# Kernel tuning notes

Hardware: AMD Instinct MI355X
Metric: run time of the kernel (lower is better)

## Reference

```python
import jax, jax.numpy as jnp
import numpy as np

EPS_LN = 1e-5

def _layernorm(x, g, b):
    mu = jnp.mean(x, axis=-1, keepdims=True)
    var = jnp.mean((x - mu) ** 2, axis=-1, keepdims=True)
    return (x - mu) * jax.lax.rsqrt(var + EPS_LN) * g + b

def _act_quant_ste(x):
    # clip_val uses detached stats -> stop_gradient
    clip_val = jax.lax.stop_gradient(
        jnp.clip(jnp.mean(jnp.abs(x), axis=-1, keepdims=True), 1e-8, None)) * 2.5
    scale = clip_val / 127.0
    x_scaled = x / scale
    x_clip = jnp.clip(x_scaled, -127.0, 127.0)
    x_q = x_scaled + jax.lax.stop_gradient(jnp.round(x_clip) - x_scaled)
    return x_q * scale

def _weight_quant_ste(w):
    scale = jax.lax.stop_gradient(jnp.clip(jnp.mean(jnp.abs(w)), 1e-8, None))
    w_norm = w / scale
    w_clip = jnp.clip(w_norm, -1.0, 1.0)
    w_q = w_norm + jax.lax.stop_gradient(jnp.round(w_clip) - w_norm)
    return w_q * scale

def _bitlinear(x, w, g, b):
    # w: [out, in]; x: [B,T,in]
    x_q = _act_quant_ste(_layernorm(x, g, b))
    w_q = _weight_quant_ste(w)
    return jnp.einsum('btd,hd->bth', x_q, w_q)

def setup_inputs() -> dict:
    D, H = 2048, 2048 * 4
    B, T = 4, 2048
    key = jax.random.key(0)
    ks = jax.random.split(key, 4)
    std = 0.02
    return {
        'x': jax.random.normal(ks[0], (B, T, D), dtype=jnp.float32),
        'mu_k': jnp.zeros((1, 1, D), jnp.float32),
        'mu_r': jnp.zeros((1, 1, D), jnp.float32),
        'wk': jax.random.normal(ks[1], (H, D), jnp.float32) * std,
        'gk': jnp.ones((D,), jnp.float32), 'bk': jnp.zeros((D,), jnp.float32),
        'wr': jax.random.normal(ks[2], (D, D), jnp.float32) * std,
        'gr': jnp.ones((D,), jnp.float32), 'br': jnp.zeros((D,), jnp.float32),
        'wv': jax.random.normal(ks[3], (D, H), jnp.float32) * std,
        'gv': jnp.ones((H,), jnp.float32), 'bv': jnp.zeros((H,), jnp.float32),
    }

def reference(x, mu_k, mu_r, wk, gk, bk, wr, gr, br, wv, gv, bv):
    B, T, C = x.shape
    prev = jnp.zeros((B, 1, C), dtype=x.dtype)  # state=None path
    x_prev = jnp.concatenate([prev, x[:, :-1, :]], axis=1)  # token shift
    dx = x_prev - x
    k_act = jax.nn.relu(_bitlinear(x + dx * mu_k, wk, gk, bk)) ** 2  # [B,T,H]
    rgate = jax.nn.sigmoid(_bitlinear(x + dx * mu_r, wr, gr, br))    # [B,T,D]
    out = rgate * _bitlinear(k_act, wv, gv, bv)                      # [B,T,D]
    return out, jax.lax.stop_gradient(x[:, -1:, :])
```

## Files before the change

### kernel.cpp

```cpp
#include <hip/hip_runtime.h>

#define T_LEN 2048
#define B_SZ  4
#define D_DIM 2048
#define H_DIM 8192
#define BT    (B_SZ * T_LEN)

typedef float f32x4 __attribute__((ext_vector_type(4)));
typedef int   i32x4v __attribute__((ext_vector_type(4)));
typedef int   i32x16v __attribute__((ext_vector_type(16)));
typedef unsigned short ushort8 __attribute__((ext_vector_type(8)));

__device__ __forceinline__ float bf2f(unsigned short u) {
    unsigned int i = ((unsigned int)u) << 16;
    return __builtin_bit_cast(float, i);
}
__device__ __forceinline__ unsigned short f2bf(float f) {
    unsigned int i = __builtin_bit_cast(unsigned int, f);
    i += 0x7fffu + ((i >> 16) & 1u);
    return (unsigned short)(i >> 16);
}

__device__ __forceinline__ float block_sum(float v, float* red) {
    #pragma unroll
    for (int o = 32; o > 0; o >>= 1) v += __shfl_down(v, o, 64);
    const int lane = threadIdx.x & 63, w = threadIdx.x >> 6;
    if (lane == 0) red[w] = v;
    __syncthreads();
    float r = red[0] + red[1] + red[2] + red[3];
    __syncthreads();
    return r;
}

__global__ void wabs_all(const float* __restrict__ wk, const float* __restrict__ wr,
                         const float* __restrict__ wv, float* __restrict__ part) {
    __shared__ float red[16];
    const int m = blockIdx.x >> 10;
    const int blk = blockIdx.x & 1023;
    const float* w = (m == 0) ? wk : (m == 1) ? wr : wv;
    const int n = (m == 1) ? D_DIM * D_DIM : H_DIM * D_DIM;
    float s = 0.f;
    int i = (blk * 256 + threadIdx.x) * 8;
    const int stride = 1024 * 256 * 8;
    for (; i < n; i += stride) {
        f32x4 a = *(const f32x4*)(w + i);
        f32x4 b = *(const f32x4*)(w + i + 4);
        #pragma unroll
        for (int j = 0; j < 4; j++) s += fabsf(a[j]) + fabsf(b[j]);
    }
    float tot = block_sum(s, red);
    if (threadIdx.x == 0) part[blockIdx.x] = tot;
}

__global__ void wfinal_all(const float* __restrict__ part, float* __restrict__ wsc) {
    __shared__ float red[16];
    const int m = blockIdx.x;
    const int n = (m == 1) ? D_DIM * D_DIM : H_DIM * D_DIM;
    float s = 0.f;
    for (int i = threadIdx.x; i < 1024; i += 256) s += part[m * 1024 + i];
    float tot = block_sum(s, red);
    if (threadIdx.x == 0) wsc[m] = fmaxf(tot / (float)n, 1e-8f);
}

__global__ void wquant_all(const float* __restrict__ wk, const float* __restrict__ wr,
                           const float* __restrict__ wv,
                           signed char* __restrict__ qk, signed char* __restrict__ qr,
                           signed char* __restrict__ qv,
                           const float* __restrict__ wsc) {
    const int b = blockIdx.x;
    int m, blk, nblk;
    if (b < 2048)      { m = 0; blk = b;        nblk = 2048; }
    else if (b < 3072) { m = 1; blk = b - 2048; nblk = 1024; }
    else               { m = 2; blk = b - 3072; nblk = 2048; }
    const float* w = (m == 0) ? wk : (m == 1) ? wr : wv;
    signed char* q = (m == 0) ? qk : (m == 1) ? qr : qv;
    const int n = (m == 1) ? D_DIM * D_DIM : H_DIM * D_DIM;
    const float s = wsc[m];
    int i = (blk * 256 + threadIdx.x) * 16;
    const int stride = nblk * 256 * 16;
    for (; i < n; i += stride) {
        union { signed char c[16]; i32x4v v; } pk;
        #pragma unroll
        for (int h = 0; h < 4; h++) {
            f32x4 a = *(const f32x4*)(w + i + h * 4);
            #pragma unroll
            for (int j = 0; j < 4; j++)
                pk.c[h * 4 + j] =
                    (signed char)(int)rintf(fminf(fmaxf(a[j] / s, -1.f), 1.f));
        }
        *(i32x4v*)(q + i) = pk.v;
    }
}

__device__ __forceinline__ void ln_quant8(const float* xm_in,
                                          const float* __restrict__ g,
                                          const float* __restrict__ b,
                                          signed char* qrow, float* srow, float* red) {
    const int base = threadIdx.x * 8;
    float xm[8];
    float s = 0.f;
    #pragma unroll
    for (int j = 0; j < 8; j++) { xm[j] = xm_in[j]; s += xm[j]; }
    const float mean = block_sum(s, red) * (1.f / D_DIM);
    float s2 = 0.f;
    #pragma unroll
    for (int j = 0; j < 8; j++) { float d = xm[j] - mean; s2 += d * d; }
    const float var  = block_sum(s2, red) * (1.f / D_DIM);
    const float rstd = 1.f / sqrtf(var + 1e-5f);
    f32x4 ga = *(const f32x4*)(g + base), gb = *(const f32x4*)(g + base + 4);
    f32x4 ba = *(const f32x4*)(b + base), bb2 = *(const f32x4*)(b + base + 4);
    float gg[8] = {ga[0],ga[1],ga[2],ga[3],gb[0],gb[1],gb[2],gb[3]};
    float bb[8] = {ba[0],ba[1],ba[2],ba[3],bb2[0],bb2[1],bb2[2],bb2[3]};
    float sa = 0.f;
    #pragma unroll
    for (int j = 0; j < 8; j++) {
        xm[j] = (xm[j] - mean) * rstd * gg[j] + bb[j];
        sa += fabsf(xm[j]);
    }
    const float amean = block_sum(sa, red) * (1.f / D_DIM);
    const float scale = fmaxf(amean, 1e-8f) * 2.5f / 127.0f;
    union { signed char c[8]; int2 v; } pk;
    #pragma unroll
    for (int j = 0; j < 8; j++)
        pk.c[j] = (signed char)(int)rintf(fminf(fmaxf(xm[j] / scale, -127.f), 127.f));
    *(int2*)(qrow + base) = pk.v;
    if (threadIdx.x == 0) *srow = scale;
}

__global__ void act_prep(const float* __restrict__ x,
                         const float* __restrict__ muk,
                         const float* __restrict__ gk, const float* __restrict__ bk,
                         const float* __restrict__ mur,
                         const float* __restrict__ gr, const float* __restrict__ br,
                         signed char* __restrict__ qk, float* __restrict__ sk,
                         signed char* __restrict__ qr, float* __restrict__ sr,
                         float* __restrict__ out2) {
    __shared__ float red[16];
    const int row = blockIdx.x;
    const int t = row & (T_LEN - 1);
    const int base = threadIdx.x * 8;

    float xv[8], xp[8];
    f32x4 xa = *(const f32x4*)(x + (size_t)row * D_DIM + base);
    f32x4 xb = *(const f32x4*)(x + (size_t)row * D_DIM + base + 4);
    xv[0]=xa[0]; xv[1]=xa[1]; xv[2]=xa[2]; xv[3]=xa[3];
    xv[4]=xb[0]; xv[5]=xb[1]; xv[6]=xb[2]; xv[7]=xb[3];
    if (t > 0) {
        f32x4 pa = *(const f32x4*)(x + (size_t)(row - 1) * D_DIM + base);
        f32x4 pb = *(const f32x4*)(x + (size_t)(row - 1) * D_DIM + base + 4);
        xp[0]=pa[0]; xp[1]=pa[1]; xp[2]=pa[2]; xp[3]=pa[3];
        xp[4]=pb[0]; xp[5]=pb[1]; xp[6]=pb[2]; xp[7]=pb[3];
    } else {
        #pragma unroll
        for (int j = 0; j < 8; j++) xp[j] = 0.f;
    }
    if (t == T_LEN - 1) {
        const int bb = row / T_LEN;
        *(f32x4*)(out2 + (size_t)bb * D_DIM + base)     = xa;
        *(f32x4*)(out2 + (size_t)bb * D_DIM + base + 4) = xb;
    }
    float mk[8], mr[8], xmk[8], xmr[8];
    f32x4 mka = *(const f32x4*)(muk + base), mkb = *(const f32x4*)(muk + base + 4);
    f32x4 mra = *(const f32x4*)(mur + base), mrb = *(const f32x4*)(mur + base + 4);
    mk[0]=mka[0]; mk[1]=mka[1]; mk[2]=mka[2]; mk[3]=mka[3];
    mk[4]=mkb[0]; mk[5]=mkb[1]; mk[6]=mkb[2]; mk[7]=mkb[3];
    mr[0]=mra[0]; mr[1]=mra[1]; mr[2]=mra[2]; mr[3]=mra[3];
    mr[4]=mrb[0]; mr[5]=mrb[1]; mr[6]=mrb[2]; mr[7]=mrb[3];
    #pragma unroll
    for (int j = 0; j < 8; j++) {
        const float dx = xp[j] - xv[j];
        xmk[j] = xv[j] + dx * mk[j];
        xmr[j] = xv[j] + dx * mr[j];
    }
    ln_quant8(xmk, gk, bk, qk + (size_t)row * D_DIM, sk + row, red);
    ln_quant8(xmr, gr, br, qr + (size_t)row * D_DIM, sr + row, red);
}

__global__ void lnq_v(const unsigned short* __restrict__ kact,
                      const float* __restrict__ g, const float* __restrict__ b,
                      signed char* __restrict__ qv, float* __restrict__ sv) {
    __shared__ float red[16];
    const int row = blockIdx.x;
    const int base = threadIdx.x * 32;
    const unsigned short* kr = kact + (size_t)row * H_DIM + base;

    float v[32];
    float s = 0.f;
    #pragma unroll
    for (int c = 0; c < 4; c++) {
        ushort8 a = *(const ushort8*)(kr + c * 8);
        #pragma unroll
        for (int j = 0; j < 8; j++) { v[c * 8 + j] = bf2f(a[j]); s += v[c * 8 + j]; }
    }
    const float mean = block_sum(s, red) * (1.f / H_DIM);
    float s2 = 0.f;
    #pragma unroll
    for (int j = 0; j < 32; j++) { float d = v[j] - mean; s2 += d * d; }
    const float var  = block_sum(s2, red) * (1.f / H_DIM);
    const float rstd = 1.f / sqrtf(var + 1e-5f);
    float sa = 0.f;
    #pragma unroll
    for (int c = 0; c < 8; c++) {
        f32x4 ga = *(const f32x4*)(g + base + c * 4);
        f32x4 ba = *(const f32x4*)(b + base + c * 4);
        #pragma unroll
        for (int j = 0; j < 4; j++) {
            int k = c * 4 + j;
            v[k] = (v[k] - mean) * rstd * ga[j] + ba[j];
            sa += fabsf(v[k]);
        }
    }
    const float amean = block_sum(sa, red) * (1.f / H_DIM);
    const float scale = fmaxf(amean, 1e-8f) * 2.5f / 127.0f;
    union { signed char c[32]; i32x4v v4[2]; } pk;
    #pragma unroll
    for (int j = 0; j < 32; j++)
        pk.c[j] = (signed char)(int)rintf(fminf(fmaxf(v[j] / scale, -127.f), 127.f));
    *(i32x4v*)(qv + (size_t)row * H_DIM + base)      = pk.v4[0];
    *(i32x4v*)(qv + (size_t)row * H_DIM + base + 16) = pk.v4[1];
    if (threadIdx.x == 0) sv[row] = scale;
}

template <int EP, int MT>
__global__ __launch_bounds__(512, 2) void gemmR(
    const signed char* __restrict__ A, const signed char* __restrict__ B,
    int K, int Nn, int gn,
    const float* __restrict__ sa, const float* __restrict__ swp,
    const unsigned short* __restrict__ gate_bf, float* __restrict__ out_f,
    unsigned short* __restrict__ out_bf) {
    constexpr int BM = MT * 256;
    __shared__ signed char Bs[4][128 * 64];
    const int tid = threadIdx.x;
    const int nwg = gridDim.x, q8 = nwg >> 3;
    const int swz = (blockIdx.x & 7) * q8 + (blockIdx.x >> 3);
    const int bm = swz / gn, bn = swz % gn;
    const int lane = tid & 63, wave = tid >> 6;
    const int lrow = lane & 31, lhalf = lane >> 5;
    const size_t arow0 = (size_t)bm * BM;
    const size_t brow0 = (size_t)bn * 128;
    const int NT = K >> 6;

    i32x16v acc[MT][4] = {};

    auto stageB = [&](int buf, int k0) {
        const int r = tid >> 2, sl = tid & 3;
        const signed char* g = B + (brow0 + r) * (size_t)K + k0 + ((sl ^ ((r >> 1) & 3)) * 16);
        __builtin_amdgcn_global_load_lds(
            (const __attribute__((address_space(1))) void*)g,
            (__attribute__((address_space(3))) void*)(Bs[buf] + tid * 16), 16, 0, 0);
    };
    auto loadA = [&](i32x4v (&a)[MT][2], int k0) {
        #pragma unroll
        for (int tm = 0; tm < MT; tm++)
            #pragma unroll
            for (int s = 0; s < 2; s++) {
                const int r = wave * (MT * 32) + tm * 32 + lrow;
                a[tm][s] = *(const i32x4v*)(A + (arow0 + r) * (size_t)K + k0 + (s * 2 + lhalf) * 16);
            }
    };
    auto readB = [&](const signed char* BsB, i32x4v (&b)[4][2]) {
        #pragma unroll
        for (int s = 0; s < 2; s++) {
            const int slot = s * 2 + lhalf;
            #pragma unroll
            for (int tn = 0; tn < 4; tn++) {
                const int r = tn * 32 + lrow;
                b[tn][s] = *(const i32x4v*)(BsB + r * 64 + ((slot ^ ((r >> 1) & 3)) * 16));
            }
        }
    };
    auto mfmaT = [&](i32x4v (&a)[MT][2], i32x4v (&b)[4][2]) {
        #pragma unroll
        for (int s = 0; s < 2; s++)
            #pragma unroll
            for (int tm = 0; tm < MT; tm++)
                #pragma unroll
                for (int tn = 0; tn < 4; tn++)
                    acc[tm][tn] = __builtin_amdgcn_mfma_i32_32x32x32_i8(
                        a[tm][s], b[tn][s], acc[tm][tn], 0, 0, 0);
    };

    i32x4v aE[MT][2], aO[MT][2];
    stageB(0, 0);
    loadA(aE, 0);
    stageB(1, 64);

    auto body = [&](int t, i32x4v (&cur)[MT][2], i32x4v (&nxt)[MT][2]) {
        const bool hasA = (t + 1 < NT);
        const bool hasB = (t + 2 < NT);
        if (hasA) loadA(nxt, (t + 1) << 6);
        if (hasB) stageB((t + 2) & 3, (t + 2) << 6);
        if (hasB) {
            if constexpr (MT == 2) asm volatile("s_waitcnt vmcnt(6)" ::: "memory");
            else                   asm volatile("s_waitcnt vmcnt(4)" ::: "memory");
        } else if (hasA) {
            if constexpr (MT == 2) asm volatile("s_waitcnt vmcnt(5)" ::: "memory");
            else                   asm volatile("s_waitcnt vmcnt(3)" ::: "memory");
        } else {
            asm volatile("s_waitcnt vmcnt(0)" ::: "memory");
        }
        __builtin_amdgcn_sched_barrier(0);
        __builtin_amdgcn_s_barrier();
        {
            i32x4v b[4][2];
            readB(Bs[t & 3], b);
            __builtin_amdgcn_s_setprio(1);
            mfmaT(cur, b);
            __builtin_amdgcn_s_setprio(0);
        }
    };

    for (int t = 0; t < NT; t += 2) {
        body(t, aE, aO);
        body(t + 1, aO, aE);
    }

    const float sw = *swp;
    #pragma unroll
    for (int tm = 0; tm < MT; tm++) {
        #pragma unroll
        for (int tn = 0; tn < 4; tn++) {
            #pragma unroll
            for (int rg = 0; rg < 16; rg++) {
                const int rin  = (rg & 3) + 8 * (rg >> 2) + 4 * lhalf;
                const int grow = bm * BM + wave * (MT * 32) + tm * 32 + rin;
                const int gcol = bn * 128 + tn * 32 + lrow;
                const float v = (float)acc[tm][tn][rg] * sa[grow] * sw;
                const size_t idx = (size_t)grow * Nn + gcol;
                if (EP == 0) {
                    float rv = fmaxf(v, 0.f);
                    out_bf[idx] = f2bf(rv * rv);
                } else if (EP == 1) {
                    out_bf[idx] = f2bf(1.0f / (1.0f + expf(-v)));
                } else {
                    out_f[idx] = bf2f(gate_bf[idx]) * v;
                }
            }
        }
    }
}

extern "C" void kernel_launch(void* const* d_in, const int* in_sizes, int n_in,
                              void* d_out, int out_size, void* d_ws, size_t ws_size,
                              hipStream_t stream) {
    const float* x   = (const float*)d_in[0];
    const float* muk = (const float*)d_in[1];
    const float* mur = (const float*)d_in[2];
    const float* wk  = (const float*)d_in[3];
    const float* gk  = (const float*)d_in[4];
    const float* bk  = (const float*)d_in[5];
    const float* wr  = (const float*)d_in[6];
    const float* gr  = (const float*)d_in[7];
    const float* br  = (const float*)d_in[8];
    const float* wv  = (const float*)d_in[9];
    const float* gv  = (const float*)d_in[10];
    const float* bv  = (const float*)d_in[11];

    char* wsb = (char*)d_ws;
    size_t off = 0;
    auto alloc = [&](size_t bytes) -> size_t {
        size_t p = off;
        off = (off + bytes + 255) & ~(size_t)255;
        return p;
    };
    const size_t o_wqk  = alloc((size_t)H_DIM * D_DIM);
    const size_t o_wqr  = alloc((size_t)D_DIM * D_DIM);
    const size_t o_wqv  = alloc((size_t)D_DIM * H_DIM);
    const size_t o_wsc  = alloc(64);
    const size_t o_part = alloc(3 * 1024 * sizeof(float));
    const size_t o_xqk  = alloc((size_t)BT * D_DIM);
    const size_t o_xqr  = alloc((size_t)BT * D_DIM);
    const size_t o_gate = alloc((size_t)BT * D_DIM * 2);
    const size_t o_sk   = alloc((size_t)BT * 4);
    const size_t o_sr   = alloc((size_t)BT * 4);
    const size_t fixed  = off;

    int CH = BT;
    while (CH > 512 &&
           fixed + (size_t)CH * (H_DIM + 2 * H_DIM + 4) + 8192 > ws_size)
        CH >>= 1;
    const size_t o_xqv  = alloc((size_t)CH * H_DIM);
    const size_t o_kact = alloc((size_t)CH * H_DIM * 2);
    const size_t o_sv   = alloc((size_t)CH * 4);

    signed char* wqk = (signed char*)(wsb + o_wqk);
    signed char* wqr = (signed char*)(wsb + o_wqr);
    signed char* wqv = (signed char*)(wsb + o_wqv);
    float* wsc  = (float*)(wsb + o_wsc);
    float* part = (float*)(wsb + o_part);
    signed char* xqk = (signed char*)(wsb + o_xqk);
    signed char* xqr = (signed char*)(wsb + o_xqr);
    unsigned short* gate = (unsigned short*)(wsb + o_gate);
    float* sk = (float*)(wsb + o_sk);
    float* sr = (float*)(wsb + o_sr);
    signed char* xqv = (signed char*)(wsb + o_xqv);
    unsigned short* kact = (unsigned short*)(wsb + o_kact);
    float* sv = (float*)(wsb + o_sv);

    float* outp = (float*)d_out;
    float* out2 = outp + (size_t)BT * D_DIM;

    wabs_all<<<3072, 256, 0, stream>>>(wk, wr, wv, part);
    wfinal_all<<<3, 256, 0, stream>>>(part, wsc);
    wquant_all<<<5120, 256, 0, stream>>>(wk, wr, wv, wqk, wqr, wqv, wsc);

    act_prep<<<BT, 256, 0, stream>>>(x, muk, gk, bk, mur, gr, br,
                                     xqk, sk, xqr, sr, out2);

    gemmR<1, 1><<<(BT / 256) * (D_DIM / 128), 512, 0, stream>>>(
        xqr, wqr, D_DIM, D_DIM, D_DIM / 128, sr, wsc + 1,
        (const unsigned short*)nullptr, (float*)nullptr, gate);

    for (int row0 = 0; row0 < BT; row0 += CH) {
        gemmR<0, 2><<<(CH / 512) * (H_DIM / 128), 512, 0, stream>>>(
            xqk + (size_t)row0 * D_DIM, wqk, D_DIM, H_DIM, H_DIM / 128,
            sk + row0, wsc + 0,
            (const unsigned short*)nullptr, (float*)nullptr, kact);

        lnq_v<<<CH, 256, 0, stream>>>(kact, gv, bv, xqv, sv);

        gemmR<2, 1><<<(CH / 256) * (D_DIM / 128), 512, 0, stream>>>(
            xqv, wqv, H_DIM, D_DIM, D_DIM / 128, sv, wsc + 2,
            gate + (size_t)row0 * D_DIM, outp + (size_t)row0 * D_DIM,
            (unsigned short*)nullptr);
    }
}
```

Measured before the change: 674.0 us.

## Pre-tile int8 activations for MFMA fragments and deepen GEMM K pipeline

The activation quantizers now write int8 activations into a tiled layout of 32-row by 16-byte blocks, so each GEMM wave loads its A fragments as fully contiguous 512-byte chunks instead of strided row reads. The GEMM is rewritten to stage 256-wide K slices of B into a triple-buffered shared-memory ring, prefetching the next slice and A fragments while computing the current one. The M tile drops to 256 rows for all three GEMMs, including the large K-projection that previously used 512. This cuts per-iteration barriers and improves A load coalescing, but uses more LDS per block, which may reduce occupancy, and loses the larger M tile's reuse of B for the big GEMM.

```diff
diff --git a/kernel.cpp b/kernel.cpp
--- a/kernel.cpp
+++ b/kernel.cpp
@@ -95,7 +95,8 @@
 __device__ __forceinline__ void ln_quant8(const float* xm_in,
                                           const float* __restrict__ g,
                                           const float* __restrict__ b,
-                                          signed char* qrow, float* srow, float* red) {
+                                          signed char* qbase, int row,
+                                          float* srow, float* red) {
     const int base = threadIdx.x * 8;
     float xm[8];
     float s = 0.f;
@@ -123,7 +124,9 @@
     #pragma unroll
     for (int j = 0; j < 8; j++)
         pk.c[j] = (signed char)(int)rintf(fminf(fmaxf(xm[j] / scale, -127.f), 127.f));
-    *(int2*)(qrow + base) = pk.v;
+    const size_t addr = ((size_t)(row >> 5) * (D_DIM / 16) + (threadIdx.x >> 1)) * 512
+                        + (row & 31) * 16 + (threadIdx.x & 1) * 8;
+    *(int2*)(qbase + addr) = pk.v;
     if (threadIdx.x == 0) *srow = scale;
 }
 
@@ -172,8 +175,8 @@
         xmk[j] = xv[j] + dx * mk[j];
         xmr[j] = xv[j] + dx * mr[j];
     }
-    ln_quant8(xmk, gk, bk, qk + (size_t)row * D_DIM, sk + row, red);
-    ln_quant8(xmr, gr, br, qr + (size_t)row * D_DIM, sr + row, red);
+    ln_quant8(xmk, gk, bk, qk, row, sk + row, red);
+    ln_quant8(xmr, gr, br, qr, row, sr + row, red);
 }
 
 __global__ void lnq_v(const unsigned short* __restrict__ kact,
@@ -216,125 +219,120 @@
     #pragma unroll
     for (int j = 0; j < 32; j++)
         pk.c[j] = (signed char)(int)rintf(fminf(fmaxf(v[j] / scale, -127.f), 127.f));
-    *(i32x4v*)(qv + (size_t)row * H_DIM + base)      = pk.v4[0];
-    *(i32x4v*)(qv + (size_t)row * H_DIM + base + 16) = pk.v4[1];
+    const size_t tb = ((size_t)(row >> 5) * (H_DIM / 16) + threadIdx.x * 2) * 512
+                      + (row & 31) * 16;
+    *(i32x4v*)(qv + tb)       = pk.v4[0];
+    *(i32x4v*)(qv + tb + 512) = pk.v4[1];
     if (threadIdx.x == 0) sv[row] = scale;
 }
 
-template <int EP, int MT>
-__global__ __launch_bounds__(512, 2) void gemmR(
-    const signed char* __restrict__ A, const signed char* __restrict__ B,
+template <int EP>
+__global__ __launch_bounds__(512, 2) void gemmP(
+    const signed char* __restrict__ Ap, const signed char* __restrict__ B,
     int K, int Nn, int gn,
     const float* __restrict__ sa, const float* __restrict__ swp,
     const unsigned short* __restrict__ gate_bf, float* __restrict__ out_f,
     unsigned short* __restrict__ out_bf) {
-    constexpr int BM = MT * 256;
-    __shared__ signed char Bs[4][128 * 64];
+    __shared__ signed char Bs[3 * 32768];
     const int tid = threadIdx.x;
     const int nwg = gridDim.x, q8 = nwg >> 3;
     const int swz = (blockIdx.x & 7) * q8 + (blockIdx.x >> 3);
     const int bm = swz / gn, bn = swz % gn;
     const int lane = tid & 63, wave = tid >> 6;
     const int lrow = lane & 31, lhalf = lane >> 5;
-    const size_t arow0 = (size_t)bm * BM;
+    const int KS = K >> 4;
+    const size_t rts = (size_t)(bm * 8 + wave) * KS;
     const size_t brow0 = (size_t)bn * 128;
-    const int NT = K >> 6;
-
-    i32x16v acc[MT][4] = {};
-
-    auto stageB = [&](int buf, int k0) {
+    const int NB = K >> 8;
+
+    i32x16v acc[4] = {};
+
+    auto stageB = [&](int p, int t) {
         const int r = tid >> 2, sl = tid & 3;
-        const signed char* g = B + (brow0 + r) * (size_t)K + k0 + ((sl ^ ((r >> 1) & 3)) * 16);
-        __builtin_amdgcn_global_load_lds(
-            (const __attribute__((address_space(1))) void*)g,
-            (__attribute__((address_space(3))) void*)(Bs[buf] + tid * 16), 16, 0, 0);
+        #pragma unroll
+        for (int j = 0; j < 4; j++) {
+            const signed char* g = B + (brow0 + r) * (size_t)K + (t * 256 + j * 64)
+                                   + ((sl ^ ((r >> 1) & 3)) * 16);
+            __builtin_amdgcn_global_load_lds(
+                (const __attribute__((address_space(1))) void*)g,
+                (__attribute__((address_space(3))) void*)(Bs + p * 32768 + j * 8192 + tid * 16),
+                16, 0, 0);
+        }
     };
-    auto loadA = [&](i32x4v (&a)[MT][2], int k0) {
-        #pragma unroll
-        for (int tm = 0; tm < MT; tm++)
+    auto loadA = [&](i32x4v (&a)[4][2], int t) {
+        #pragma unroll
+        for (int s = 0; s < 4; s++)
             #pragma unroll
-            for (int s = 0; s < 2; s++) {
-                const int r = wave * (MT * 32) + tm * 32 + lrow;
-                a[tm][s] = *(const i32x4v*)(A + (arow0 + r) * (size_t)K + k0 + (s * 2 + lhalf) * 16);
-            }
+            for (int sl = 0; sl < 2; sl++)
+                a[s][sl] = *(const i32x4v*)(
+                    Ap + ((rts + (size_t)(t * 16 + s * 4 + sl * 2)) << 9) + lane * 16);
     };
-    auto readB = [&](const signed char* BsB, i32x4v (&b)[4][2]) {
-        #pragma unroll
-        for (int s = 0; s < 2; s++) {
-            const int slot = s * 2 + lhalf;
+    auto readB = [&](int p, int s, i32x4v (&b)[4][2]) {
+        const signed char* basep = Bs + p * 32768 + s * 8192;
+        #pragma unroll
+        for (int sl = 0; sl < 2; sl++) {
+            const int slot = sl * 2 + lhalf;
             #pragma unroll
             for (int tn = 0; tn < 4; tn++) {
                 const int r = tn * 32 + lrow;
-                b[tn][s] = *(const i32x4v*)(BsB + r * 64 + ((slot ^ ((r >> 1) & 3)) * 16));
+                b[tn][sl] = *(const i32x4v*)(basep + r * 64 + ((slot ^ ((r >> 1) & 3)) * 16));
             }
         }
     };
-    auto mfmaT = [&](i32x4v (&a)[MT][2], i32x4v (&b)[4][2]) {
-        #pragma unroll
-        for (int s = 0; s < 2; s++)
+
+    auto bodyf = [&](int t, i32x4v (&aC)[4][2], i32x4v (&aN)[4][2]) {
+        const int p = t % 3;
+        const bool pf = (t + 1 < NB);
+        if (pf) {
+            stageB((t + 1) % 3, t + 1);
+            asm volatile("s_waitcnt vmcnt(12)" ::: "memory");
+        } else {
+            asm volatile("s_waitcnt vmcnt(8)" ::: "memory");
+        }
+        __builtin_amdgcn_sched_barrier(0);
+        __builtin_amdgcn_s_barrier();
+        __builtin_amdgcn_sched_barrier(0);
+        if (pf) loadA(aN, t + 1);
+        #pragma unroll
+        for (int s = 0; s < 4; s++) {
+            i32x4v b[4][2];
+            readB(p, s, b);
+            __builtin_amdgcn_s_setprio(1);
             #pragma unroll
-            for (int tm = 0; tm < MT; tm++)
+            for (int sl = 0; sl < 2; sl++)
                 #pragma unroll
                 for (int tn = 0; tn < 4; tn++)
-                    acc[tm][tn] = __builtin_amdgcn_mfma_i32_32x32x32_i8(
-                        a[tm][s], b[tn][s], acc[tm][tn], 0, 0, 0);
+                    acc[tn] = __builtin_amdgcn_mfma_i32_32x32x32_i8(
+                        aC[s][sl], b[tn][sl], acc[tn], 0, 0, 0);
+            __builtin_amdgcn_s_setprio(0);
+        }
     };
 
-    i32x4v aE[MT][2], aO[MT][2];
+    i32x4v aE[4][2], aO[4][2];
     stageB(0, 0);
     loadA(aE, 0);
-    stageB(1, 64);
-
-    auto body = [&](int t, i32x4v (&cur)[MT][2], i32x4v (&nxt)[MT][2]) {
-        const bool hasA = (t + 1 < NT);
-        const bool hasB = (t + 2 < NT);
-        if (hasA) loadA(nxt, (t + 1) << 6);
-        if (hasB) stageB((t + 2) & 3, (t + 2) << 6);
-        if (hasB) {
-            if constexpr (MT == 2) asm volatile("s_waitcnt vmcnt(6)" ::: "memory");
-            else                   asm volatile("s_waitcnt vmcnt(4)" ::: "memory");
-        } else if (hasA) {
-            if constexpr (MT == 2) asm volatile("s_waitcnt vmcnt(5)" ::: "memory");
-            else                   asm volatile("s_waitcnt vmcnt(3)" ::: "memory");
-        } else {
-            asm volatile("s_waitcnt vmcnt(0)" ::: "memory");
-        }
-        __builtin_amdgcn_sched_barrier(0);
-        __builtin_amdgcn_s_barrier();
-        {
-            i32x4v b[4][2];
-            readB(Bs[t & 3], b);
-            __builtin_amdgcn_s_setprio(1);
-            mfmaT(cur, b);
-            __builtin_amdgcn_s_setprio(0);
-        }
-    };
-
-    for (int t = 0; t < NT; t += 2) {
-        body(t, aE, aO);
-        body(t + 1, aO, aE);
+    for (int t = 0; t < NB; t += 2) {
+        bodyf(t, aE, aO);
+        bodyf(t + 1, aO, aE);
     }
 
     const float sw = *swp;
     #pragma unroll
-    for (int tm = 0; tm < MT; tm++) {
-        #pragma unroll
-        for (int tn = 0; tn < 4; tn++) {
-            #pragma unroll
-            for (int rg = 0; rg < 16; rg++) {
-                const int rin  = (rg & 3) + 8 * (rg >> 2) + 4 * lhalf;
-                const int grow = bm * BM + wave * (MT * 32) + tm * 32 + rin;
-                const int gcol = bn * 128 + tn * 32 + lrow;
-                const float v = (float)acc[tm][tn][rg] * sa[grow] * sw;
-                const size_t idx = (size_t)grow * Nn + gcol;
-                if (EP == 0) {
-                    float rv = fmaxf(v, 0.f);
-                    out_bf[idx] = f2bf(rv * rv);
-                } else if (EP == 1) {
-                    out_bf[idx] = f2bf(1.0f / (1.0f + expf(-v)));
-                } else {
-                    out_f[idx] = bf2f(gate_bf[idx]) * v;
-                }
+    for (int tn = 0; tn < 4; tn++) {
+        #pragma unroll
+        for (int rg = 0; rg < 16; rg++) {
+            const int rin  = (rg & 3) + 8 * (rg >> 2) + 4 * lhalf;
+            const int grow = bm * 256 + wave * 32 + rin;
+            const int gcol = bn * 128 + tn * 32 + lrow;
+            const float v = (float)acc[tn][rg] * sa[grow] * sw;
+            const size_t idx = (size_t)grow * Nn + gcol;
+            if (EP == 0) {
+                float rv = fmaxf(v, 0.f);
+                out_bf[idx] = f2bf(rv * rv);
+            } else if (EP == 1) {
+                out_bf[idx] = f2bf(1.0f / (1.0f + expf(-v)));
+            } else {
+                out_f[idx] = bf2f(gate_bf[idx]) * v;
             }
         }
     }
@@ -407,19 +405,19 @@
     act_prep<<<BT, 256, 0, stream>>>(x, muk, gk, bk, mur, gr, br,
                                      xqk, sk, xqr, sr, out2);
 
-    gemmR<1, 1><<<(BT / 256) * (D_DIM / 128), 512, 0, stream>>>(
+    gemmP<1><<<(BT / 256) * (D_DIM / 128), 512, 0, stream>>>(
         xqr, wqr, D_DIM, D_DIM, D_DIM / 128, sr, wsc + 1,
         (const unsigned short*)nullptr, (float*)nullptr, gate);
 
     for (int row0 = 0; row0 < BT; row0 += CH) {
-        gemmR<0, 2><<<(CH / 512) * (H_DIM / 128), 512, 0, stream>>>(
+        gemmP<0><<<(CH / 256) * (H_DIM / 128), 512, 0, stream>>>(
             xqk + (size_t)row0 * D_DIM, wqk, D_DIM, H_DIM, H_DIM / 128,
             sk + row0, wsc + 0,
             (const unsigned short*)nullptr, (float*)nullptr, kact);
 
         lnq_v<<<CH, 256, 0, stream>>>(kact, gv, bv, xqv, sv);
 
-        gemmR<2, 1><<<(CH / 256) * (D_DIM / 128), 512, 0, stream>>>(
+        gemmP<2><<<(CH / 256) * (D_DIM / 128), 512, 0, stream>>>(
             xqv, wqv, H_DIM, D_DIM, D_DIM / 128, sv, wsc + 2,
             gate + (size_t)row0 * D_DIM, outp + (size_t)row0 * D_DIM,
             (unsigned short*)nullptr);
```

Result: faster. 600.5 us, median of 2 (-10.9%).
